# Performance work log

Measured on AMD Instinct MI355X. Metric: run time of the kernel, lower is better.

## Reference

```python
import jax, jax.numpy as jnp
import numpy as np

B, D, E, TOP_K = 16384, 2048, 8, 2


def setup_inputs() -> dict:
    key = jax.random.key(0)
    ks = jax.random.split(key, 5)
    scale = 1.0 / np.sqrt(D)
    x = jax.random.normal(ks[0], (B, D), dtype=jnp.float32)
    # expert Linear(D, D) weights/biases, stacked over experts
    expert_w = jax.random.uniform(ks[1], (E, D, D), minval=-scale, maxval=scale, dtype=jnp.float32)
    expert_b = jax.random.uniform(ks[2], (E, D), minval=-scale, maxval=scale, dtype=jnp.float32)
    # gate Linear(D, E)
    gate_w = jax.random.uniform(ks[3], (D, E), minval=-scale, maxval=scale, dtype=jnp.float32)
    gate_b = jax.random.uniform(ks[4], (E,), minval=-scale, maxval=scale, dtype=jnp.float32)
    return {"x": x, "expert_w": expert_w, "expert_b": expert_b, "gate_w": gate_w, "gate_b": gate_b}


def reference(x, expert_w, expert_b, gate_w, gate_b):
    # gate logits: (B, E)
    logits = x @ gate_w + gate_b
    topk_logits, topk_idx = jax.lax.top_k(logits, TOP_K)          # (B, K)
    topk_weights = jax.nn.softmax(topk_logits, axis=-1)           # (B, K)
    # dense: compute every expert for every token (faithful to original)
    expert_outputs = jax.nn.relu(
        jnp.einsum("bd,edf->bef", x, expert_w) + expert_b[None, :, :]
    )                                                             # (B, E, D); dropout is identity in eval mode
    # gather the top-k experts per token
    selected = jnp.take_along_axis(expert_outputs, topk_idx[:, :, None], axis=1)  # (B, K, D)
    out = jnp.sum(selected * topk_weights[:, :, None], axis=1)    # (B, D)
    return out
```

## Files before the change

### kernel.cpp

```cpp
#include <hip/hip_runtime.h>
#include <hip/hip_bf16.h>
#include <math.h>

#define NB 16384
#define DD 2048
#define NE 8
#define TM 128
#define TN 128
#define BK 64
#define NT_TILES (DD / TN)
#define MT_PER_PASS (NB / TM + NE)
#define GEMM_GRID (MT_PER_PASS * NT_TILES)
#define BPX (GEMM_GRID / 8)

typedef float f32x4 __attribute__((ext_vector_type(4)));
typedef short bf16x8 __attribute__((ext_vector_type(8)));

__device__ __forceinline__ short f2bf(float f) {
  union { float f; unsigned u; } v; v.f = f;
  unsigned r = (v.u + 0x7FFFu + ((v.u >> 16) & 1u)) >> 16;
  return (short)r;
}

__device__ __forceinline__ void gload16(const void* g, void* l) {
  __builtin_amdgcn_global_load_lds((const __attribute__((address_space(1))) void*)g,
                                   (__attribute__((address_space(3))) void*)l,
                                   16, 0, 0);
}

__global__ void conv_x(const float* __restrict__ x, short* __restrict__ xb) {
  size_t i = ((size_t)blockIdx.x * 256 + threadIdx.x) * 8;
  f32x4 a = *(const f32x4*)(x + i);
  f32x4 b = *(const f32x4*)(x + i + 4);
  bf16x8 o;
  o[0] = f2bf(a[0]); o[1] = f2bf(a[1]); o[2] = f2bf(a[2]); o[3] = f2bf(a[3]);
  o[4] = f2bf(b[0]); o[5] = f2bf(b[1]); o[6] = f2bf(b[2]); o[7] = f2bf(b[3]);
  *(bf16x8*)(xb + i) = o;
}

__global__ void conv_wT(const float* __restrict__ w, short* __restrict__ wt) {
  __shared__ float tile[64][68];
  int bid = blockIdx.x;
  int e = bid >> 10;
  int tt = bid & 1023;
  int d0 = (tt >> 5) << 6;
  int f0 = (tt & 31) << 6;
  const float* we = w + (size_t)e * DD * DD;
  int t = threadIdx.x;
  int col = (t & 15) << 2;
#pragma unroll
  for (int p = 0; p < 4; ++p) {
    int dl = (t >> 4) + p * 16;
    f32x4 v = *(const f32x4*)(we + (size_t)(d0 + dl) * DD + f0 + col);
    *(f32x4*)&tile[dl][col] = v;
  }
  __syncthreads();
  int fl = t >> 2;
  int ds = (t & 3) << 4;
  short tmp[16];
#pragma unroll
  for (int j = 0; j < 16; ++j) tmp[j] = f2bf(tile[ds + j][fl]);
  short* dst = wt + (size_t)e * DD * DD + (size_t)(f0 + fl) * DD + d0 + ds;
  *(bf16x8*)dst = *(const bf16x8*)tmp;
  *(bf16x8*)(dst + 8) = *(const bf16x8*)(tmp + 8);
}

__global__ void gate_topk(const float* __restrict__ x, const float* __restrict__ gw,
                          const float* __restrict__ gb, int* __restrict__ ridx,
                          float* __restrict__ rw) {
  int wid = threadIdx.x >> 6;
  int lane = threadIdx.x & 63;
  int b = blockIdx.x * 4 + wid;
  const float* xr = x + (size_t)b * DD;
  double acc[8];
#pragma unroll
  for (int e = 0; e < 8; ++e) acc[e] = 0.0;
  for (int d = lane; d < DD; d += 64) {
    float xv = xr[d];
    f32x4 g0 = *(const f32x4*)(gw + d * 8);
    f32x4 g1 = *(const f32x4*)(gw + d * 8 + 4);
    double xd = (double)xv;
    acc[0] += xd * g0[0]; acc[1] += xd * g0[1];
    acc[2] += xd * g0[2]; acc[3] += xd * g0[3];
    acc[4] += xd * g1[0]; acc[5] += xd * g1[1];
    acc[6] += xd * g1[2]; acc[7] += xd * g1[3];
  }
#pragma unroll
  for (int off = 32; off > 0; off >>= 1) {
#pragma unroll
    for (int e = 0; e < 8; ++e) acc[e] += __shfl_down(acc[e], off);
  }
  if (lane == 0) {
    double l[8];
#pragma unroll
    for (int e = 0; e < 8; ++e) l[e] = acc[e] + (double)gb[e];
    int i0 = 0;
#pragma unroll
    for (int e = 1; e < 8; ++e) if (l[e] > l[i0]) i0 = e;
    int i1 = (i0 == 0) ? 1 : 0;
#pragma unroll
    for (int e = 0; e < 8; ++e) if (e != i0 && l[e] > l[i1]) i1 = e;
    double z = exp(l[i1] - l[i0]);
    float w0 = (float)(1.0 / (1.0 + z));
    float w1 = (float)(z / (1.0 + z));
    ridx[2 * b] = i0; ridx[2 * b + 1] = i1;
    rw[2 * b] = w0;   rw[2 * b + 1] = w1;
  }
}

__global__ void hist_tok(const int* __restrict__ ridx, int* __restrict__ partials) {
  __shared__ int h[16];
  int t = threadIdx.x;
  if (t < 16) h[t] = 0;
  __syncthreads();
  int t0 = blockIdx.x * 512;
  for (int i = t; i < 512; i += 256) {
    int tok = t0 + i;
    atomicAdd(&h[ridx[2 * tok]], 1);
    atomicAdd(&h[8 + ridx[2 * tok + 1]], 1);
  }
  __syncthreads();
  if (t < 16) partials[blockIdx.x * 16 + t] = h[t];
}

__global__ void scan_small(const int* __restrict__ partials, int* __restrict__ base,
                           int* __restrict__ cnts, int* __restrict__ offs) {
  __shared__ int c[16], o[16];
  int j = threadIdx.x;
  if (j < 16) {
    int s = 0;
    for (int b = 0; b < 32; ++b) s += partials[b * 16 + j];
    c[j] = s; cnts[j] = s;
  }
  __syncthreads();
  if (j < 2) {
    int a = 0;
    for (int e = 0; e < 8; ++e) { o[j * 8 + e] = a; a += c[j * 8 + e]; }
  }
  __syncthreads();
  if (j < 16) {
    int r = o[j];
    offs[j] = o[j];
    for (int b = 0; b < 32; ++b) { base[b * 16 + j] = r; r += partials[b * 16 + j]; }
  }
}

__global__ void scatter_tok(const int* __restrict__ ridx, const float* __restrict__ rw,
                            const int* __restrict__ base,
                            int* __restrict__ lists0, float* __restrict__ elw0,
                            int* __restrict__ lists1, float* __restrict__ elw1) {
  __shared__ int h[16];
  int t = threadIdx.x;
  if (t < 16) h[t] = 0;
  __syncthreads();
  int t0 = blockIdx.x * 512;
  const int* bb = base + blockIdx.x * 16;
  for (int i = t; i < 512; i += 256) {
    int tok = t0 + i;
    int e0 = ridx[2 * tok], e1 = ridx[2 * tok + 1];
    int r0 = atomicAdd(&h[e0], 1);
    int r1 = atomicAdd(&h[8 + e1], 1);
    int p0 = bb[e0] + r0;
    int p1 = bb[8 + e1] + r1;
    lists0[p0] = tok; elw0[p0] = rw[2 * tok];
    lists1[p1] = tok; elw1[p1] = rw[2 * tok + 1];
  }
}

template <int ADD>
__global__ __launch_bounds__(256)
void moe_gemm(const short* __restrict__ xb, const short* __restrict__ wt,
              const float* __restrict__ eb, const int* __restrict__ cnts,
              const int* __restrict__ offs, const int* __restrict__ lists,
              const float* __restrict__ elw, float* __restrict__ out) {
  __shared__ short As[TM * BK];
  __shared__ short Bs[TN * BK];

  int bid = blockIdx.x;
  int swz = (bid & 7) * BPX + (bid >> 3);
  int mt = swz % MT_PER_PASS;
  int nt = swz / MT_PER_PASS;

  int e = 0, cnt = 0;
  for (; e < NE; ++e) {
    cnt = cnts[e];
    int te = (cnt + TM - 1) >> 7;
    if (mt < te) break;
    mt -= te;
  }
  if (e >= NE) return;

  int m0 = mt * TM;
  int n0 = nt * TN;
  int off_e = offs[e];
  int tid = threadIdx.x;
  int lane = tid & 63, wid = tid >> 6;
  int wr = wid >> 1, wc = wid & 1;

  int srow = tid >> 3;
  int scol = (((tid & 7) ^ (srow & 7)) << 3);
  const short* asrc[4];
  const short* bsrc[4];
#pragma unroll
  for (int p = 0; p < 4; ++p) {
    int r = srow + p * 32;
    int gr = m0 + r;
    int tok = lists[off_e + ((gr < cnt) ? gr : (cnt - 1))];
    asrc[p] = xb + (size_t)tok * DD + scol;
    bsrc[p] = wt + ((size_t)e * DD + (size_t)(n0 + r)) * DD + scol;
  }
  int ldsbase = wid * 512;

  f32x4 acc[4][4];
#pragma unroll
  for (int i = 0; i < 4; ++i)
#pragma unroll
    for (int j = 0; j < 4; ++j) acc[i][j] = (f32x4){0.f, 0.f, 0.f, 0.f};

  int lrow = lane & 15;
  int lk = (lane >> 4) << 3;
  int x7 = (lrow & 7) << 3;

  for (int k0 = 0; k0 < DD; k0 += BK) {
#pragma unroll
    for (int p = 0; p < 4; ++p) {
      gload16(asrc[p] + k0, &As[p * 2048 + ldsbase]);
      gload16(bsrc[p] + k0, &Bs[p * 2048 + ldsbase]);
    }
    __syncthreads();
#pragma unroll
    for (int kk = 0; kk < 2; ++kk) {
      int pcol = ((kk * 32 + lk) ^ x7);
      bf16x8 af[4], bfr[4];
#pragma unroll
      for (int i = 0; i < 4; ++i)
        af[i] = *(const bf16x8*)&As[(wr * 64 + i * 16 + lrow) * BK + pcol];
#pragma unroll
      for (int j = 0; j < 4; ++j)
        bfr[j] = *(const bf16x8*)&Bs[(wc * 64 + j * 16 + lrow) * BK + pcol];
#pragma unroll
      for (int i = 0; i < 4; ++i)
#pragma unroll
        for (int j = 0; j < 4; ++j)
          acc[i][j] = __builtin_amdgcn_mfma_f32_16x16x32_bf16(af[i], bfr[j], acc[i][j], 0, 0, 0);
    }
    __syncthreads();
  }

  int r0 = (lane >> 4) << 2;
#pragma unroll
  for (int i = 0; i < 4; ++i) {
    int mloc = wr * 64 + i * 16 + r0;
#pragma unroll
    for (int r = 0; r < 4; ++r) {
      int gr = m0 + mloc + r;
      if (gr >= cnt) continue;
      int tok = lists[off_e + gr];
      float wgt = elw[off_e + gr];
      float* orow = out + (size_t)tok * DD;
#pragma unroll
      for (int j = 0; j < 4; ++j) {
        int n = n0 + wc * 64 + j * 16 + lrow;
        float v = acc[i][j][r] + eb[e * DD + n];
        v = fmaxf(v, 0.f) * wgt;
        if (ADD) v += __builtin_nontemporal_load(&orow[n]);
        __builtin_nontemporal_store(v, &orow[n]);
      }
    }
  }
}

extern "C" void kernel_launch(void* const* d_in, const int* in_sizes, int n_in,
                              void* d_out, int out_size, void* d_ws, size_t ws_size,
                              hipStream_t stream) {
  const float* x   = (const float*)d_in[0];
  const float* ewt = (const float*)d_in[1];
  const float* eb  = (const float*)d_in[2];
  const float* gw  = (const float*)d_in[3];
  const float* gb  = (const float*)d_in[4];
  float* out = (float*)d_out;

  char* ws = (char*)d_ws;
  short* xb      = (short*)(ws);
  short* wt      = (short*)(ws + 67108864);
  int*   ridx    = (int*)  (ws + 134217728);
  float* rw      = (float*)(ws + 134348800);
  int*   lists0  = (int*)  (ws + 134479872);
  float* elw0    = (float*)(ws + 134545408);
  int*   lists1  = (int*)  (ws + 134610944);
  float* elw1    = (float*)(ws + 134676480);
  int*   partials= (int*)  (ws + 134742016);
  int*   base    = (int*)  (ws + 134744064);
  int*   cnts    = (int*)  (ws + 134746112);
  int*   offs    = (int*)  (ws + 134746176);

  conv_x<<<(NB * DD / 8) / 256, 256, 0, stream>>>(x, xb);
  conv_wT<<<NE * 32 * 32, 256, 0, stream>>>(ewt, wt);
  gate_topk<<<NB / 4, 256, 0, stream>>>(x, gw, gb, ridx, rw);
  hist_tok<<<32, 256, 0, stream>>>(ridx, partials);
  scan_small<<<1, 64, 0, stream>>>(partials, base, cnts, offs);
  scatter_tok<<<32, 256, 0, stream>>>(ridx, rw, base, lists0, elw0, lists1, elw1);
  moe_gemm<0><<<GEMM_GRID, 256, 0, stream>>>(xb, wt, eb, cnts,     offs,     lists0, elw0, out);
  moe_gemm<1><<<GEMM_GRID, 256, 0, stream>>>(xb, wt, eb, cnts + 8, offs + 8, lists1, elw1, out);
}
```

Baseline: 645.5 us.

## Rewrite MoE GEMM as 256x256 double-buffered 8-wave pipeline, fuse x conversion into gate

The grouped GEMM moves from 128x128 tiles with 4 waves and a single LDS buffer to 256x256 tiles with 8 waves. LDS is now double-buffered and the K loop is split into phases that interleave global-to-LDS loads with MFMA work, using explicit waitcnt, barriers and setprio. The bf16 conversion of x is folded into the gate/top-k kernel so x is read once. The block swizzle is dropped. Larger tiles mean more padding waste per expert and higher register and LDS use per block, which can lower occupancy.

```diff
diff --git a/kernel.cpp b/kernel.cpp
--- a/kernel.cpp
+++ b/kernel.cpp
@@ -5,13 +5,14 @@
 #define NB 16384
 #define DD 2048
 #define NE 8
-#define TM 128
-#define TN 128
+#define TM 256
+#define TN 256
 #define BK 64
+#define NKT (DD / BK)
+#define NIT (NKT / 2)
+#define MT_PER_PASS (NB / TM + NE)
 #define NT_TILES (DD / TN)
-#define MT_PER_PASS (NB / TM + NE)
 #define GEMM_GRID (MT_PER_PASS * NT_TILES)
-#define BPX (GEMM_GRID / 8)
 
 typedef float f32x4 __attribute__((ext_vector_type(4)));
 typedef short bf16x8 __attribute__((ext_vector_type(8)));
@@ -26,16 +27,6 @@
   __builtin_amdgcn_global_load_lds((const __attribute__((address_space(1))) void*)g,
                                    (__attribute__((address_space(3))) void*)l,
                                    16, 0, 0);
-}
-
-__global__ void conv_x(const float* __restrict__ x, short* __restrict__ xb) {
-  size_t i = ((size_t)blockIdx.x * 256 + threadIdx.x) * 8;
-  f32x4 a = *(const f32x4*)(x + i);
-  f32x4 b = *(const f32x4*)(x + i + 4);
-  bf16x8 o;
-  o[0] = f2bf(a[0]); o[1] = f2bf(a[1]); o[2] = f2bf(a[2]); o[3] = f2bf(a[3]);
-  o[4] = f2bf(b[0]); o[5] = f2bf(b[1]); o[6] = f2bf(b[2]); o[7] = f2bf(b[3]);
-  *(bf16x8*)(xb + i) = o;
 }
 
 __global__ void conv_wT(const float* __restrict__ w, short* __restrict__ wt) {
@@ -65,25 +56,37 @@
   *(bf16x8*)(dst + 8) = *(const bf16x8*)(tmp + 8);
 }
 
-__global__ void gate_topk(const float* __restrict__ x, const float* __restrict__ gw,
-                          const float* __restrict__ gb, int* __restrict__ ridx,
-                          float* __restrict__ rw) {
+__global__ void gate_conv(const float* __restrict__ x, const float* __restrict__ gw,
+                          const float* __restrict__ gb, short* __restrict__ xb,
+                          int* __restrict__ ridx, float* __restrict__ rw) {
   int wid = threadIdx.x >> 6;
   int lane = threadIdx.x & 63;
   int b = blockIdx.x * 4 + wid;
   const float* xr = x + (size_t)b * DD;
+  short* xbr = xb + (size_t)b * DD;
   double acc[8];
 #pragma unroll
   for (int e = 0; e < 8; ++e) acc[e] = 0.0;
-  for (int d = lane; d < DD; d += 64) {
-    float xv = xr[d];
-    f32x4 g0 = *(const f32x4*)(gw + d * 8);
-    f32x4 g1 = *(const f32x4*)(gw + d * 8 + 4);
-    double xd = (double)xv;
-    acc[0] += xd * g0[0]; acc[1] += xd * g0[1];
-    acc[2] += xd * g0[2]; acc[3] += xd * g0[3];
-    acc[4] += xd * g1[0]; acc[5] += xd * g1[1];
-    acc[6] += xd * g1[2]; acc[7] += xd * g1[3];
+#pragma unroll
+  for (int it = 0; it < 4; ++it) {
+    int d8 = (it * 64 + lane) * 8;
+    f32x4 a = *(const f32x4*)(xr + d8);
+    f32x4 c = *(const f32x4*)(xr + d8 + 4);
+    bf16x8 o;
+    o[0] = f2bf(a[0]); o[1] = f2bf(a[1]); o[2] = f2bf(a[2]); o[3] = f2bf(a[3]);
+    o[4] = f2bf(c[0]); o[5] = f2bf(c[1]); o[6] = f2bf(c[2]); o[7] = f2bf(c[3]);
+    *(bf16x8*)(xbr + d8) = o;
+#pragma unroll
+    for (int j = 0; j < 8; ++j) {
+      float xv = (j < 4) ? a[j] : c[j - 4];
+      double xd = (double)xv;
+      f32x4 g0 = *(const f32x4*)(gw + (size_t)(d8 + j) * 8);
+      f32x4 g1 = *(const f32x4*)(gw + (size_t)(d8 + j) * 8 + 4);
+      acc[0] += xd * g0[0]; acc[1] += xd * g0[1];
+      acc[2] += xd * g0[2]; acc[3] += xd * g0[3];
+      acc[4] += xd * g1[0]; acc[5] += xd * g1[1];
+      acc[6] += xd * g1[2]; acc[7] += xd * g1[3];
+    }
   }
 #pragma unroll
   for (int off = 32; off > 0; off >>= 1) {
@@ -167,24 +170,65 @@
   }
 }
 
+#define VMCNT2 asm volatile("s_waitcnt vmcnt(2)" ::: "memory")
+#define VMCNT0 asm volatile("s_waitcnt vmcnt(0)" ::: "memory")
+#define NOWAIT ((void)0)
+
+#define STAGE_A(buf, h, kt) {                                                  \
+  gload16(aptr[h][0] + (size_t)(kt) * 64, &As[(buf)*16384 + (h)*8192 + tid*8]);\
+  gload16(aptr[h][1] + (size_t)(kt) * 64, &As[(buf)*16384 + (h)*8192 + 4096 + tid*8]); }
+
+#define STAGE_B(buf, h, kt) {                                                  \
+  gload16(bptr[h][0] + (size_t)(kt) * 64, &Bs[(buf)*16384 + (h)*8192 + tid*8]);\
+  gload16(bptr[h][1] + (size_t)(kt) * 64, &Bs[(buf)*16384 + (h)*8192 + 4096 + tid*8]); }
+
+#define READ_A(buf, mh)                                                        \
+  _Pragma("unroll") for (int i4 = 0; i4 < 4; ++i4) {                           \
+    af[i4][0] = *(const bf16x8*)&As[(buf)*16384 + arow + ((mh)*64 + i4*16)*64 + csw0]; \
+    af[i4][1] = *(const bf16x8*)&As[(buf)*16384 + arow + ((mh)*64 + i4*16)*64 + csw1]; }
+
+#define READ_B(buf, nh)                                                        \
+  _Pragma("unroll") for (int j2 = 0; j2 < 2; ++j2) {                           \
+    bf[j2][0] = *(const bf16x8*)&Bs[(buf)*16384 + brow + ((nh)*32 + j2*16)*64 + csw0]; \
+    bf[j2][1] = *(const bf16x8*)&Bs[(buf)*16384 + brow + ((nh)*32 + j2*16)*64 + csw1]; }
+
+#define MFMA16(mh, nh)                                                         \
+  _Pragma("unroll") for (int i4 = 0; i4 < 4; ++i4)                             \
+  _Pragma("unroll") for (int j2 = 0; j2 < 2; ++j2) {                           \
+    acc[(mh)*4+i4][(nh)*2+j2] = __builtin_amdgcn_mfma_f32_16x16x32_bf16(       \
+        af[i4][0], bf[j2][0], acc[(mh)*4+i4][(nh)*2+j2], 0, 0, 0);             \
+    acc[(mh)*4+i4][(nh)*2+j2] = __builtin_amdgcn_mfma_f32_16x16x32_bf16(       \
+        af[i4][1], bf[j2][1], acc[(mh)*4+i4][(nh)*2+j2], 0, 0, 0); }
+
+#define PHASE(buf, mh, nh, DO_RA, DO_RB, STAGE_STMT, WAIT_STMT) {              \
+  if (DO_RA) { READ_A(buf, mh); }                                              \
+  if (DO_RB) { READ_B(buf, nh); }                                              \
+  STAGE_STMT;                                                                  \
+  WAIT_STMT;                                                                   \
+  __builtin_amdgcn_s_barrier();                                                \
+  asm volatile("s_waitcnt lgkmcnt(0)" ::: "memory");                           \
+  __builtin_amdgcn_sched_barrier(0);                                           \
+  __builtin_amdgcn_s_setprio(1);                                               \
+  MFMA16(mh, nh);                                                              \
+  __builtin_amdgcn_s_setprio(0);                                               \
+  __builtin_amdgcn_s_barrier(); }
+
 template <int ADD>
-__global__ __launch_bounds__(256)
+__global__ __launch_bounds__(512, 2)
 void moe_gemm(const short* __restrict__ xb, const short* __restrict__ wt,
               const float* __restrict__ eb, const int* __restrict__ cnts,
               const int* __restrict__ offs, const int* __restrict__ lists,
               const float* __restrict__ elw, float* __restrict__ out) {
-  __shared__ short As[TM * BK];
-  __shared__ short Bs[TN * BK];
-
-  int bid = blockIdx.x;
-  int swz = (bid & 7) * BPX + (bid >> 3);
-  int mt = swz % MT_PER_PASS;
-  int nt = swz / MT_PER_PASS;
+  __shared__ short As[2 * 16384];
+  __shared__ short Bs[2 * 16384];
+
+  int nt = blockIdx.x & 7;
+  int mt = blockIdx.x >> 3;
 
   int e = 0, cnt = 0;
   for (; e < NE; ++e) {
     cnt = cnts[e];
-    int te = (cnt + TM - 1) >> 7;
+    int te = (cnt + TM - 1) >> 8;
     if (mt < te) break;
     mt -= te;
   }
@@ -195,62 +239,64 @@
   int off_e = offs[e];
   int tid = threadIdx.x;
   int lane = tid & 63, wid = tid >> 6;
-  int wr = wid >> 1, wc = wid & 1;
-
-  int srow = tid >> 3;
-  int scol = (((tid & 7) ^ (srow & 7)) << 3);
-  const short* asrc[4];
-  const short* bsrc[4];
-#pragma unroll
-  for (int p = 0; p < 4; ++p) {
-    int r = srow + p * 32;
-    int gr = m0 + r;
-    int tok = lists[off_e + ((gr < cnt) ? gr : (cnt - 1))];
-    asrc[p] = xb + (size_t)tok * DD + scol;
-    bsrc[p] = wt + ((size_t)e * DD + (size_t)(n0 + r)) * DD + scol;
-  }
-  int ldsbase = wid * 512;
-
-  f32x4 acc[4][4];
-#pragma unroll
-  for (int i = 0; i < 4; ++i)
+  int wr = wid >> 2, wc = wid & 3;
+
+  int trow = tid >> 3;
+  int scol = ((tid & 7) ^ (trow & 7)) << 3;
+  const short* aptr[2][2];
+  const short* bptr[2][2];
+#pragma unroll
+  for (int h = 0; h < 2; ++h)
+#pragma unroll
+    for (int l = 0; l < 2; ++l) {
+      int r = h * 128 + l * 64 + trow;
+      int gr = m0 + r;
+      int tok = lists[off_e + ((gr < cnt) ? gr : (cnt - 1))];
+      aptr[h][l] = xb + (size_t)tok * DD + scol;
+      bptr[h][l] = wt + ((size_t)e * DD + (size_t)(n0 + r)) * DD + scol;
+    }
+
+  int lane15 = lane & 15;
+  int csw0 = (((lane >> 4)    ) ^ (lane & 7)) << 3;
+  int csw1 = (((lane >> 4) + 4) ^ (lane & 7)) << 3;
+  int arow = (wr * 128 + lane15) * 64;
+  int brow = (wc * 64  + lane15) * 64;
+
+  f32x4 acc[8][4];
+#pragma unroll
+  for (int i = 0; i < 8; ++i)
 #pragma unroll
     for (int j = 0; j < 4; ++j) acc[i][j] = (f32x4){0.f, 0.f, 0.f, 0.f};
 
-  int lrow = lane & 15;
-  int lk = (lane >> 4) << 3;
-  int x7 = (lrow & 7) << 3;
-
-  for (int k0 = 0; k0 < DD; k0 += BK) {
-#pragma unroll
-    for (int p = 0; p < 4; ++p) {
-      gload16(asrc[p] + k0, &As[p * 2048 + ldsbase]);
-      gload16(bsrc[p] + k0, &Bs[p * 2048 + ldsbase]);
-    }
-    __syncthreads();
-#pragma unroll
-    for (int kk = 0; kk < 2; ++kk) {
-      int pcol = ((kk * 32 + lk) ^ x7);
-      bf16x8 af[4], bfr[4];
-#pragma unroll
-      for (int i = 0; i < 4; ++i)
-        af[i] = *(const bf16x8*)&As[(wr * 64 + i * 16 + lrow) * BK + pcol];
-#pragma unroll
-      for (int j = 0; j < 4; ++j)
-        bfr[j] = *(const bf16x8*)&Bs[(wc * 64 + j * 16 + lrow) * BK + pcol];
-#pragma unroll
-      for (int i = 0; i < 4; ++i)
-#pragma unroll
-        for (int j = 0; j < 4; ++j)
-          acc[i][j] = __builtin_amdgcn_mfma_f32_16x16x32_bf16(af[i], bfr[j], acc[i][j], 0, 0, 0);
-    }
-    __syncthreads();
-  }
-
+  bf16x8 af[4][2], bf[2][2];
+
+  STAGE_A(0, 0, 0); STAGE_A(0, 1, 0); STAGE_B(0, 0, 0); STAGE_B(0, 1, 0);
+  STAGE_A(1, 0, 1);
+  VMCNT2;
+  __builtin_amdgcn_s_barrier();
+
+  for (int i = 0; i < NIT; ++i) {
+    int t2 = 2 * i + 2, t3 = 2 * i + 3;
+    PHASE(0, 0, 0, 1, 1, STAGE_A(1, 1, 2 * i + 1), NOWAIT);
+    PHASE(0, 0, 1, 0, 1, STAGE_B(1, 0, 2 * i + 1), NOWAIT);
+    PHASE(0, 1, 1, 1, 0, STAGE_B(1, 1, 2 * i + 1), NOWAIT);
+    if (t2 < NKT) { PHASE(0, 1, 0, 0, 1, STAGE_A(0, 0, t2), VMCNT2); }
+    else          { PHASE(0, 1, 0, 0, 1, NOWAIT,            VMCNT0); }
+    PHASE(1, 0, 0, 1, 1, if (t2 < NKT) STAGE_A(0, 1, t2), NOWAIT);
+    PHASE(1, 0, 1, 0, 1, if (t2 < NKT) STAGE_B(0, 0, t2), NOWAIT);
+    PHASE(1, 1, 1, 1, 0, if (t2 < NKT) STAGE_B(0, 1, t2), NOWAIT);
+    if (t3 < NKT) { PHASE(1, 1, 0, 0, 1, STAGE_A(1, 0, t3), VMCNT2); }
+    else          { PHASE(1, 1, 0, 0, 1, NOWAIT,            VMCNT0); }
+  }
+
+  float ebv[4];
+#pragma unroll
+  for (int j4 = 0; j4 < 4; ++j4)
+    ebv[j4] = eb[e * DD + n0 + wc * 64 + j4 * 16 + lane15];
   int r0 = (lane >> 4) << 2;
 #pragma unroll
-  for (int i = 0; i < 4; ++i) {
-    int mloc = wr * 64 + i * 16 + r0;
+  for (int i8 = 0; i8 < 8; ++i8) {
+    int mloc = wr * 128 + i8 * 16 + r0;
 #pragma unroll
     for (int r = 0; r < 4; ++r) {
       int gr = m0 + mloc + r;
@@ -259,9 +305,9 @@
       float wgt = elw[off_e + gr];
       float* orow = out + (size_t)tok * DD;
 #pragma unroll
-      for (int j = 0; j < 4; ++j) {
-        int n = n0 + wc * 64 + j * 16 + lrow;
-        float v = acc[i][j][r] + eb[e * DD + n];
+      for (int j4 = 0; j4 < 4; ++j4) {
+        int n = n0 + wc * 64 + j4 * 16 + lane15;
+        float v = acc[i8][j4][r] + ebv[j4];
         v = fmaxf(v, 0.f) * wgt;
         if (ADD) v += __builtin_nontemporal_load(&orow[n]);
         __builtin_nontemporal_store(v, &orow[n]);
@@ -294,12 +340,11 @@
   int*   cnts    = (int*)  (ws + 134746112);
   int*   offs    = (int*)  (ws + 134746176);
 
-  conv_x<<<(NB * DD / 8) / 256, 256, 0, stream>>>(x, xb);
   conv_wT<<<NE * 32 * 32, 256, 0, stream>>>(ewt, wt);
-  gate_topk<<<NB / 4, 256, 0, stream>>>(x, gw, gb, ridx, rw);
+  gate_conv<<<NB / 4, 256, 0, stream>>>(x, gw, gb, xb, ridx, rw);
   hist_tok<<<32, 256, 0, stream>>>(ridx, partials);
   scan_small<<<1, 64, 0, stream>>>(partials, base, cnts, offs);
   scatter_tok<<<32, 256, 0, stream>>>(ridx, rw, base, lists0, elw0, lists1, elw1);
-  moe_gemm<0><<<GEMM_GRID, 256, 0, stream>>>(xb, wt, eb, cnts,     offs,     lists0, elw0, out);
-  moe_gemm<1><<<GEMM_GRID, 256, 0, stream>>>(xb, wt, eb, cnts + 8, offs + 8, lists1, elw1, out);
-}
+  moe_gemm<0><<<GEMM_GRID, 512, 0, stream>>>(xb, wt, eb, cnts,     offs,     lists0, elw0, out);
+  moe_gemm<1><<<GEMM_GRID, 512, 0, stream>>>(xb, wt, eb, cnts + 8, offs + 8, lists1, elw1, out);
+}
```

Result: slower. 680.8 us (+5.5%).
